# Performance work log

Measured on AMD Instinct MI355X. Metric: run time of the kernel, lower is better.

## Reference

```python
import jax, jax.numpy as jnp
import numpy as np
import math

HID, NH, NKV, HD = 2048, 16, 4, 128
GROUPS = NH // NKV
ROPE_THETA = 10000.0
NBITS = 8


def fake_quant(x, n_bits=NBITS):
    """Per-tensor symmetric min-max fake quantization with STE."""
    qmax = float(2 ** (n_bits - 1) - 1)
    scale = jnp.maximum(jnp.max(jnp.abs(x)) / qmax, jnp.asarray(1e-8, x.dtype))
    q = jnp.clip(jnp.round(x / scale), -qmax - 1.0, qmax) * scale
    return x + jax.lax.stop_gradient(q - x)


def quant_linear(x, w):
    # QuantLinear: fake-quant activation and weight, then x @ w.T
    return jnp.einsum('bsh,oh->bso', fake_quant(x), fake_quant(w))


def rope_cos_sin(position_ids, head_dim, dtype):
    inv_freq = 1.0 / (ROPE_THETA ** (jnp.arange(0, head_dim, 2, dtype=jnp.float32) / head_dim))
    freqs = position_ids.astype(jnp.float32)[..., None] * inv_freq  # [B,S,hd/2]
    emb = jnp.concatenate([freqs, freqs], axis=-1)                   # [B,S,hd]
    return jnp.cos(emb).astype(dtype), jnp.sin(emb).astype(dtype)


def rotate_half(x):
    h = x.shape[-1] // 2
    return jnp.concatenate([-x[..., h:], x[..., :h]], axis=-1)


def setup_inputs() -> dict:
    key = jax.random.key(0)
    ks = jax.random.split(key, 6)
    B, S = 2, 2048
    hidden_states = jax.random.normal(ks[0], (B, S, HID), dtype=jnp.float32)
    neg = jnp.finfo(jnp.float32).min
    causal = jnp.where(jnp.tril(jnp.ones((S, S), dtype=bool)), 0.0, neg).astype(jnp.float32)
    attention_mask = jnp.broadcast_to(causal[None, None], (B, 1, S, S))
    position_ids = jnp.broadcast_to(jnp.arange(S, dtype=jnp.int64)[None], (B, S))
    wq = jax.random.normal(ks[1], (NH * HD, HID), dtype=jnp.float32) * 0.02
    wk = jax.random.normal(ks[2], (NKV * HD, HID), dtype=jnp.float32) * 0.02
    wv = jax.random.normal(ks[3], (NKV * HD, HID), dtype=jnp.float32) * 0.02
    wo = jax.random.normal(ks[4], (HID, NH * HD), dtype=jnp.float32) * 0.02
    return {"hidden_states": hidden_states, "attention_mask": attention_mask,
            "position_ids": position_ids, "wq": wq, "wk": wk, "wv": wv, "wo": wo}


def reference(hidden_states, attention_mask, position_ids, wq, wk, wv, wo):
    B, S, _ = hidden_states.shape
    dtype = hidden_states.dtype
    # quantized projections -> [B, nH, S, hd] / [B, nKV, S, hd]
    q = quant_linear(hidden_states, wq).reshape(B, S, NH, HD).transpose(0, 2, 1, 3)
    k = quant_linear(hidden_states, wk).reshape(B, S, NKV, HD).transpose(0, 2, 1, 3)
    v = quant_linear(hidden_states, wv).reshape(B, S, NKV, HD).transpose(0, 2, 1, 3)
    # RoPE
    cos, sin = rope_cos_sin(position_ids, HD, dtype)
    cos, sin = cos[:, None], sin[:, None]  # broadcast over heads
    q = q * cos + rotate_half(q) * sin
    k = k * cos + rotate_half(k) * sin
    # repeat_kv (GQA)
    k = jnp.repeat(k, GROUPS, axis=1)
    v = jnp.repeat(v, GROUPS, axis=1)
    # fake-quantized QK^T
    q = fake_quant(q)
    k = fake_quant(k)
    attn_weights = jnp.einsum('bhqd,bhkd->bhqk', q, k) / math.sqrt(HD)
    attn_weights = attn_weights + attention_mask
    attn_weights = jnp.maximum(attn_weights, jnp.finfo(attn_weights.dtype).min)
    attn_weights = jax.nn.softmax(attn_weights.astype(jnp.float32), axis=-1).astype(dtype)
    # fake-quantized PV
    p = fake_quant(attn_weights)
    v = fake_quant(v)
    attn_output = jnp.einsum('bhqk,bhkd->bhqd', p, v)
    attn_output = attn_output.transpose(0, 2, 1, 3).reshape(B, S, NH * HD)
    return quant_linear(attn_output, wo)
```

## Files before the change

### kernel.cpp

```cpp
#include <hip/hip_runtime.h>
#include <math.h>
#include <stdint.h>
#include <stddef.h>

#define HID 2048
#define NH 16
#define NKV 4
#define HD 128
#define GROUPS (NH / NKV)
#define BATCH 2
#define SEQ 2048

#define N_HS  8388608ull
#define N_Q   8388608ull
#define N_KV  2097152ull
#define N_WQ  4194304ull
#define N_WKV 1048576ull
#define N_WO  4194304ull

typedef __attribute__((ext_vector_type(8))) short bf16x8;
typedef __attribute__((ext_vector_type(4))) float f32x4;

__device__ inline float quantv(float x, float s) {
  float q = rintf(x / s);
  return fminf(fmaxf(q, -128.0f), 127.0f);
}

__device__ inline float slot_scale(const unsigned int* slots, int i) {
  return fmaxf(__uint_as_float(slots[i]) / 127.0f, 1e-8f);
}

__device__ inline unsigned short f2bf(float x) {
  return (unsigned short)(__float_as_uint(x) >> 16);
}

__device__ inline float amax4(float4 v) {
  return fmaxf(fmaxf(fabsf(v.x), fabsf(v.y)), fmaxf(fabsf(v.z), fabsf(v.w)));
}

__device__ inline void block_amax_atomic(float m, unsigned int* slot) {
  __shared__ float red[256];
  red[threadIdx.x] = m;
  __syncthreads();
  for (int o = 128; o > 0; o >>= 1) {
    if (threadIdx.x < o) red[threadIdx.x] = fmaxf(red[threadIdx.x], red[threadIdx.x + o]);
    __syncthreads();
  }
  if (threadIdx.x == 0) atomicMax(slot, __float_as_uint(red[0]));
}

__device__ __forceinline__ void gload_lds16(const void* g, void* l) {
  __builtin_amdgcn_global_load_lds((const __attribute__((address_space(1))) unsigned int*)g,
                                   (__attribute__((address_space(3))) unsigned int*)l, 16, 0, 0);
}

__global__ __launch_bounds__(256) void absmax5_k(const float* __restrict__ a0,
                                                 const float* __restrict__ a1,
                                                 const float* __restrict__ a2,
                                                 const float* __restrict__ a3,
                                                 const float* __restrict__ a4,
                                                 unsigned int* __restrict__ slots) {
  const int t = blockIdx.y;
  const float* x = t == 0 ? a0 : t == 1 ? a1 : t == 2 ? a2 : t == 3 ? a3 : a4;
  const size_t n4 = (t == 0 ? N_HS : t == 1 ? N_WQ : t == 2 ? N_WKV : t == 3 ? N_WKV : N_WO) / 4;
  const float4* xp = (const float4*)x;
  float m = 0.0f;
  for (size_t i = (size_t)blockIdx.x * 256 + threadIdx.x; i < n4; i += (size_t)gridDim.x * 256)
    m = fmaxf(m, amax4(xp[i]));
  block_amax_atomic(m, slots + t);
}

__global__ __launch_bounds__(256) void quant5_k(const float* __restrict__ a0,
                                                const float* __restrict__ a1,
                                                const float* __restrict__ a2,
                                                const float* __restrict__ a3,
                                                const float* __restrict__ a4,
                                                const unsigned int* __restrict__ slots,
                                                unsigned short* __restrict__ o0,
                                                unsigned short* __restrict__ o1,
                                                unsigned short* __restrict__ o2,
                                                unsigned short* __restrict__ o3,
                                                unsigned short* __restrict__ o4) {
  const int t = blockIdx.y;
  const float* x = t == 0 ? a0 : t == 1 ? a1 : t == 2 ? a2 : t == 3 ? a3 : a4;
  unsigned short* o = t == 0 ? o0 : t == 1 ? o1 : t == 2 ? o2 : t == 3 ? o3 : o4;
  const size_t n4 = (t == 0 ? N_HS : t == 1 ? N_WQ : t == 2 ? N_WKV : t == 3 ? N_WKV : N_WO) / 4;
  const float s = fmaxf(__uint_as_float(slots[t]) / 127.0f, 1e-8f);
  const float4* xp = (const float4*)x;
  ushort4* op = (ushort4*)o;
  for (size_t i = (size_t)blockIdx.x * 256 + threadIdx.x; i < n4; i += (size_t)gridDim.x * 256) {
    float4 v = xp[i];
    ushort4 r;
    r.x = f2bf(quantv(v.x, s));
    r.y = f2bf(quantv(v.y, s));
    r.z = f2bf(quantv(v.z, s));
    r.w = f2bf(quantv(v.w, s));
    op[i] = r;
  }
}

__global__ __launch_bounds__(256) void quant2_k(const float* __restrict__ a0,
                                                const float* __restrict__ a1,
                                                const unsigned int* __restrict__ slots,
                                                unsigned short* __restrict__ o0,
                                                unsigned short* __restrict__ o1) {
  const int t = blockIdx.y;
  const float* x = t == 0 ? a0 : a1;
  unsigned short* o = t == 0 ? o0 : o1;
  const size_t n4 = (t == 0 ? N_Q : N_KV) / 4;
  const float s = fmaxf(__uint_as_float(slots[5 + t]) / 127.0f, 1e-8f);
  const float4* xp = (const float4*)x;
  ushort4* op = (ushort4*)o;
  for (size_t i = (size_t)blockIdx.x * 256 + threadIdx.x; i < n4; i += (size_t)gridDim.x * 256) {
    float4 v = xp[i];
    ushort4 r;
    r.x = f2bf(quantv(v.x, s));
    r.y = f2bf(quantv(v.y, s));
    r.z = f2bf(quantv(v.z, s));
    r.w = f2bf(quantv(v.w, s));
    op[i] = r;
  }
}

__global__ __launch_bounds__(256) void quant1_k(const float* __restrict__ x, size_t n4,
                                                const unsigned int* __restrict__ slot,
                                                unsigned short* __restrict__ out) {
  const float s = fmaxf(__uint_as_float(*slot) / 127.0f, 1e-8f);
  const float4* xp = (const float4*)x;
  ushort4* op = (ushort4*)out;
  for (size_t i = (size_t)blockIdx.x * 256 + threadIdx.x; i < n4; i += (size_t)gridDim.x * 256) {
    float4 v = xp[i];
    ushort4 r;
    r.x = f2bf(quantv(v.x, s));
    r.y = f2bf(quantv(v.y, s));
    r.z = f2bf(quantv(v.z, s));
    r.w = f2bf(quantv(v.w, s));
    op[i] = r;
  }
}

__global__ __launch_bounds__(256) void vtq_k(const float* __restrict__ vbuf,
                                             const unsigned int* __restrict__ slots,
                                             unsigned short* __restrict__ vbt) {
  __shared__ unsigned short L[128 * 72];
  const int tid = threadIdx.x;
  const int s0 = blockIdx.x * 64;
  const int hk = blockIdx.y;
  const int b = blockIdx.z;
  const float s = fmaxf(__uint_as_float(slots[7]) / 127.0f, 1e-8f);
#pragma unroll
  for (int it = 0; it < 8; it++) {
    int idx = tid + it * 256;
    int sl = idx >> 5, c4 = idx & 31;
    float4 v = ((const float4*)(vbuf + ((size_t)(b * SEQ + s0 + sl) * NKV + hk) * HD))[c4];
    L[(c4 * 4 + 0) * 72 + sl] = f2bf(quantv(v.x, s));
    L[(c4 * 4 + 1) * 72 + sl] = f2bf(quantv(v.y, s));
    L[(c4 * 4 + 2) * 72 + sl] = f2bf(quantv(v.z, s));
    L[(c4 * 4 + 3) * 72 + sl] = f2bf(quantv(v.w, s));
  }
  __syncthreads();
  const size_t obase = ((size_t)(b * NKV + hk)) * HD * SEQ + s0;
#pragma unroll
  for (int it = 0; it < 4; it++) {
    int idx = tid + it * 256;
    int d = idx >> 3, sc = idx & 7;
    *(bf16x8*)(vbt + obase + (size_t)d * SEQ + sc * 8) = *(const bf16x8*)(&L[d * 72 + sc * 8]);
  }
}

__device__ __forceinline__ void gemm_body(const unsigned short* __restrict__ A,
                                          const unsigned short* __restrict__ B,
                                          float* __restrict__ C, int N, int K, int m0, int n0,
                                          float sc, int amax_slot, unsigned int* slots) {
  __shared__ unsigned short As[3][128 * 32];
  __shared__ unsigned short Bs[3][128 * 32];
  const int tid = threadIdx.x;
  const int wave = tid >> 6, lane = tid & 63;
  const int l16 = lane & 15, quad = lane >> 4;
  const int wm = (wave & 1) * 64, wn = (wave >> 1) * 64;

  f32x4 acc[4][4];
#pragma unroll
  for (int i = 0; i < 4; i++)
#pragma unroll
    for (int j = 0; j < 4; j++) acc[i][j] = (f32x4){0.f, 0.f, 0.f, 0.f};

  auto STAGE = [&](int buf, int kt) {
#pragma unroll
    for (int it = 0; it < 2; it++) {
      int c = it * 256 + tid;
      int r = c >> 2, kc = (c & 3) * 8;
      gload_lds16(A + (size_t)(m0 + r) * K + kt + kc, &As[buf][(it * 256 + wave * 64) * 8]);
      gload_lds16(B + (size_t)(n0 + r) * K + kt + kc, &Bs[buf][(it * 256 + wave * 64) * 8]);
    }
  };

  const int nk = K / 32;
  STAGE(0, 0);
  STAGE(1, 32);
  STAGE(2, 64);
  for (int t = 0; t < nk; t++) {
    const int buf = t % 3;
    if (t + 3 < nk + 1)      asm volatile("s_waitcnt vmcnt(8)" ::: "memory");
    else if (t + 2 < nk + 1) asm volatile("s_waitcnt vmcnt(4)" ::: "memory");
    else                     asm volatile("s_waitcnt vmcnt(0)" ::: "memory");
    __builtin_amdgcn_sched_barrier(0);
    __builtin_amdgcn_s_barrier();
    __builtin_amdgcn_sched_barrier(0);
    bf16x8 af[4], bq[4];
#pragma unroll
    for (int i = 0; i < 4; i++)
      af[i] = *(const bf16x8*)(&As[buf][(wm + i * 16 + l16) * 32 + quad * 8]);
#pragma unroll
    for (int j = 0; j < 4; j++)
      bq[j] = *(const bf16x8*)(&Bs[buf][(wn + j * 16 + l16) * 32 + quad * 8]);
    asm volatile("s_waitcnt lgkmcnt(0)" ::: "memory");
    __builtin_amdgcn_sched_barrier(0);
    __builtin_amdgcn_s_barrier();
    __builtin_amdgcn_sched_barrier(0);
    if (t + 3 < nk) STAGE(buf, (t + 3) * 32);
#pragma unroll
    for (int i = 0; i < 4; i++)
#pragma unroll
      for (int j = 0; j < 4; j++)
        acc[i][j] = __builtin_amdgcn_mfma_f32_16x16x32_bf16(af[i], bq[j], acc[i][j], 0, 0, 0);
  }

  float am = 0.0f;
#pragma unroll
  for (int i = 0; i < 4; i++)
#pragma unroll
    for (int j = 0; j < 4; j++)
#pragma unroll
      for (int r = 0; r < 4; r++) {
        int row = m0 + wm + i * 16 + quad * 4 + r;
        int col = n0 + wn + j * 16 + l16;
        float v = acc[i][j][r] * sc;
        C[(size_t)row * N + col] = v;
        am = fmaxf(am, fabsf(v));
      }
  if (amax_slot >= 0) {
    __syncthreads();
    float* red = (float*)As;
    red[tid] = am;
    __syncthreads();
    for (int o = 128; o > 0; o >>= 1) {
      if (tid < o) red[tid] = fmaxf(red[tid], red[tid + o]);
      __syncthreads();
    }
    if (tid == 0) atomicMax(slots + amax_slot, __float_as_uint(red[0]));
  }
}

__global__ __launch_bounds__(256) void gemm_qkv_k(const unsigned short* __restrict__ A,
                                                  const unsigned short* __restrict__ Bq,
                                                  const unsigned short* __restrict__ Bk,
                                                  const unsigned short* __restrict__ Bv,
                                                  float* __restrict__ Cq, float* __restrict__ Ck,
                                                  float* __restrict__ Cv,
                                                  unsigned int* __restrict__ slots) {
  const int nt = blockIdx.x, m0 = blockIdx.y * 128;
  const unsigned short* B;
  float* C;
  int N, n0, ib, amx;
  if (nt < 16) {
    B = Bq; C = Cq; N = 2048; n0 = nt * 128; ib = 1; amx = -1;
  } else if (nt < 20) {
    B = Bk; C = Ck; N = 512; n0 = (nt - 16) * 128; ib = 2; amx = -1;
  } else {
    B = Bv; C = Cv; N = 512; n0 = (nt - 20) * 128; ib = 3; amx = 7;
  }
  const float sc = slot_scale(slots, 0) * slot_scale(slots, ib);
  gemm_body(A, B, C, N, HID, m0, n0, sc, amx, slots);
}

__global__ __launch_bounds__(256) void gemm_o_k(const unsigned short* __restrict__ A,
                                                const unsigned short* __restrict__ B,
                                                float* __restrict__ C,
                                                unsigned int* __restrict__ slots) {
  const float sc = slot_scale(slots, 8) * slot_scale(slots, 4);
  gemm_body(A, B, C, HID, NH * HD, blockIdx.y * 128, blockIdx.x * 128, sc, -1, slots);
}

__global__ __launch_bounds__(256) void rope_table_k(float2* __restrict__ tab) {
  int idx = blockIdx.x * 256 + threadIdx.x;
  int i = idx & 63, s = idx >> 6;
  float inv = 1.0f / powf(10000.0f, (float)(2 * i) * (1.0f / 128.0f));
  float fr = (float)s * inv;
  tab[idx] = make_float2(cosf(fr), sinf(fr));
}

__global__ __launch_bounds__(256) void rope_kernel(float* __restrict__ t, int nh, int nhs,
                                                   const float2* __restrict__ tab,
                                                   unsigned int* __restrict__ slot) {
  const size_t total4 = (size_t)BATCH * SEQ * nh * 16;
  float am = 0.0f;
  for (size_t it = (size_t)blockIdx.x * 256 + threadIdx.x; it < total4;
       it += (size_t)gridDim.x * 256) {
    const int i4 = (int)(it & 15);
    const int h = (int)((it >> 4) & (nh - 1));
    const int s = (int)((it >> (4 + nhs)) & (SEQ - 1));
    const int b = (int)(it >> (15 + nhs));
    const size_t base = ((size_t)(b * SEQ + s) * nh + h) * HD + i4 * 4;
    float4 x1 = *(const float4*)(t + base);
    float4 x2 = *(const float4*)(t + base + 64);
    const float4* tp = (const float4*)(tab + (s << 6) + i4 * 4);
    float4 cs01 = tp[0];
    float4 cs23 = tp[1];
    float4 r1, r2;
    r1.x = x1.x * cs01.x - x2.x * cs01.y;  r2.x = x2.x * cs01.x + x1.x * cs01.y;
    r1.y = x1.y * cs01.z - x2.y * cs01.w;  r2.y = x2.y * cs01.z + x1.y * cs01.w;
    r1.z = x1.z * cs23.x - x2.z * cs23.y;  r2.z = x2.z * cs23.x + x1.z * cs23.y;
    r1.w = x1.w * cs23.z - x2.w * cs23.w;  r2.w = x2.w * cs23.z + x1.w * cs23.w;
    *(float4*)(t + base) = r1;
    *(float4*)(t + base + 64) = r2;
    am = fmaxf(am, fmaxf(amax4(r1), amax4(r2)));
  }
  block_amax_atomic(am, slot);
}

#define TK 64
#define KS_STRIDE (HD + 8)
#define VT_STRIDE (TK + 8)
#define PS_STRIDE (TK + 8)

__device__ __forceinline__ void ldK(bf16x8 r[4], const unsigned short* kb, int b, int hk,
                                    int j0, int tid) {
#pragma unroll
  for (int it = 0; it < 4; it++) {
    int c2 = tid + it * 256;
    int rr = c2 >> 4, c = c2 & 15;
    r[it] = *(const bf16x8*)(kb + ((size_t)(b * SEQ + j0 + rr) * NKV + hk) * HD + c * 8);
  }
}
__device__ __forceinline__ void stK(unsigned short* Ks, const bf16x8 r[4], int tid) {
#pragma unroll
  for (int it = 0; it < 4; it++) {
    int c2 = tid + it * 256;
    int rr = c2 >> 4, c = c2 & 15;
    *(bf16x8*)(&Ks[rr * KS_STRIDE + c * 8]) = r[it];
  }
}
__device__ __forceinline__ void ldV(bf16x8 r[4], const unsigned short* vbt, size_t vbase,
                                    int j0, int tid) {
#pragma unroll
  for (int it = 0; it < 4; it++) {
    int idx = tid + it * 256;
    int d = idx >> 3, sc = idx & 7;
    r[it] = *(const bf16x8*)(vbt + vbase + (size_t)d * SEQ + j0 + sc * 8);
  }
}
__device__ __forceinline__ void stV(unsigned short* Vt, const bf16x8 r[4], int tid) {
#pragma unroll
  for (int it = 0; it < 4; it++) {
    int idx = tid + it * 256;
    int d = idx >> 3, sc = idx & 7;
    *(bf16x8*)(&Vt[d * VT_STRIDE + sc * 8]) = r[it];
  }
}

__device__ __forceinline__ void qk4_pair(f32x4 sfrA[4], f32x4 sfrB[4], const unsigned short* Ks,
                                         const bf16x8 qfA[4], const bf16x8 qfB[4], bool doA,
                                         int l16, int quad) {
#pragma unroll
  for (int kt = 0; kt < 4; kt++) {
    f32x4 aA = {0.f, 0.f, 0.f, 0.f}, aB = {0.f, 0.f, 0.f, 0.f};
    const unsigned short* kp = &Ks[(kt * 16 + l16) * KS_STRIDE + quad * 8];
#pragma unroll
    for (int s = 0; s < 4; s++) {
      bf16x8 kf = *(const bf16x8*)(kp + s * 32);
      if (doA) aA = __builtin_amdgcn_mfma_f32_16x16x32_bf16(qfA[s], kf, aA, 0, 0, 0);
      aB = __builtin_amdgcn_mfma_f32_16x16x32_bf16(qfB[s], kf, aB, 0, 0, 0);
    }
    sfrA[kt] = aA;
    sfrB[kt] = aB;
  }
}
__device__ __forceinline__ void lacc(float l[4], const f32x4 sfr[4], float ss, bool diag,
                                     int j0, int qrb, int l16) {
  if (!diag) {
#pragma unroll
    for (int kt = 0; kt < 4; kt++)
#pragma unroll
      for (int r = 0; r < 4; r++) l[r] += __expf(fminf(sfr[kt][r] * ss, 80.0f));
  } else {
#pragma unroll
    for (int kt = 0; kt < 4; kt++) {
      const int key = j0 + kt * 16 + l16;
#pragma unroll
      for (int r = 0; r < 4; r++) {
        float e = __expf(fminf(sfr[kt][r] * ss, 80.0f));
        l[r] += (key <= qrb + r) ? e : 0.0f;
      }
    }
  }
}
__device__ __forceinline__ void pquant(unsigned short* Psb, const f32x4 sfr[4],
                                       const float il[4], float ss, bool diag, int j0,
                                       int qrb, int wave, int l16, int quad) {
  if (!diag) {
#pragma unroll
    for (int kt = 0; kt < 4; kt++)
#pragma unroll
      for (int r = 0; r < 4; r++) {
        float e = __expf(fminf(sfr[kt][r] * ss, 80.0f));
        float p = fminf(rintf(e * il[r]), 127.0f);
        Psb[(wave * 16 + quad * 4 + r) * PS_STRIDE + kt * 16 + l16] = f2bf(p);
      }
  } else {
#pragma unroll
    for (int kt = 0; kt < 4; kt++) {
      const int key = j0 + kt * 16 + l16;
#pragma unroll
      for (int r = 0; r < 4; r++) {
        float e = __expf(fminf(sfr[kt][r] * ss, 80.0f));
        float p = (key <= qrb + r) ? fminf(rintf(e * il[r]), 127.0f) : 0.0f;
        Psb[(wave * 16 + quad * 4 + r) * PS_STRIDE + kt * 16 + l16] = f2bf(p);
      }
    }
  }
}
__device__ __forceinline__ void pvacc_pair(f32x4 ofA[8], f32x4 ofB[8], const unsigned short* Ps,
                                           const unsigned short* Vt, bool doA, int wave,
                                           int l16, int quad) {
  const unsigned short* ppA = &Ps[(wave * 16 + l16) * PS_STRIDE + quad * 8];
  const unsigned short* ppB = ppA + 64 * PS_STRIDE;
  bf16x8 pA0, pA1;
  if (doA) {
    pA0 = *(const bf16x8*)ppA;
    pA1 = *(const bf16x8*)(ppA + 32);
  }
  bf16x8 pB0 = *(const bf16x8*)ppB;
  bf16x8 pB1 = *(const bf16x8*)(ppB + 32);
#pragma unroll
  for (int n = 0; n < 8; n++) {
    const unsigned short* vp = &Vt[(n * 16 + l16) * VT_STRIDE + quad * 8];
    bf16x8 v0 = *(const bf16x8*)vp;
    bf16x8 v1 = *(const bf16x8*)(vp + 32);
    ofB[n] = __builtin_amdgcn_mfma_f32_16x16x32_bf16(pB0, v0, ofB[n], 0, 0, 0);
    ofB[n] = __builtin_amdgcn_mfma_f32_16x16x32_bf16(pB1, v1, ofB[n], 0, 0, 0);
    if (doA) {
      ofA[n] = __builtin_amdgcn_mfma_f32_16x16x32_bf16(pA0, v0, ofA[n], 0, 0, 0);
      ofA[n] = __builtin_amdgcn_mfma_f32_16x16x32_bf16(pA1, v1, ofA[n], 0, 0, 0);
    }
  }
}

__global__ __launch_bounds__(256, 2) void attn_mfma_kernel(const unsigned short* __restrict__ qb,
                                                           const unsigned short* __restrict__ kb,
                                                           const unsigned short* __restrict__ vbt,
                                                           float* __restrict__ ob,
                                                           unsigned int* __restrict__ slots) {
  __shared__ unsigned short Ks[TK * KS_STRIDE];
  __shared__ unsigned short Vt[HD * VT_STRIDE];
  __shared__ unsigned short Ps[128 * PS_STRIDE];

  const int tid = threadIdx.x;
  const int wave = tid >> 6;
  const int lane = tid & 63;
  const int l16 = lane & 15;
  const int quad = lane >> 4;
  const int id = blockIdx.x;
  const int b = (id & 7) >> 2;
  const int hk = id & 3;
  const int j = id >> 3;
  const int h = hk * GROUPS + (j & 3);
  const int slot = j >> 2;
  const int q0A = slot * 64, ntA = slot + 1;
  const int q0B = (31 - slot) * 64, ntB = 32 - slot;

  const float s_q = slot_scale(slots, 5);
  const float s_k = slot_scale(slots, 6);
  const float s_v = slot_scale(slots, 7);
  const float ss = s_q * s_k / 11.313708498984761f;
  const float scale_p = 1.0f / 127.0f;
  const size_t vbase = ((size_t)(b * NKV + hk)) * HD * SEQ;

  bf16x8 qfA[4], qfB[4];
  {
    const unsigned short* qpA =
        qb + ((size_t)(b * SEQ + q0A + wave * 16 + l16) * NH + h) * HD + quad * 8;
    const unsigned short* qpB =
        qb + ((size_t)(b * SEQ + q0B + wave * 16 + l16) * NH + h) * HD + quad * 8;
#pragma unroll
    for (int s = 0; s < 4; s++) {
      qfA[s] = *(const bf16x8*)(qpA + s * 32);
      qfB[s] = *(const bf16x8*)(qpB + s * 32);
    }
  }
  const int qrbA = q0A + wave * 16 + quad * 4;
  const int qrbB = q0B + wave * 16 + quad * 4;

  float lA[4] = {0.f, 0.f, 0.f, 0.f}, lB[4] = {0.f, 0.f, 0.f, 0.f};
  bf16x8 kreg[4];
  ldK(kreg, kb, b, hk, 0, tid);
  for (int t = 0; t < ntB; t++) {
    const int j0 = t * TK;
    __syncthreads();
    stK(Ks, kreg, tid);
    if (t + 1 < ntB) ldK(kreg, kb, b, hk, (t + 1) * TK, tid);
    __syncthreads();
    const bool doA = (t < ntA);
    f32x4 sfrA[4], sfrB[4];
    qk4_pair(sfrA, sfrB, Ks, qfA, qfB, doA, l16, quad);
    if (doA) lacc(lA, sfrA, ss, t == ntA - 1, j0, qrbA, l16);
    lacc(lB, sfrB, ss, t == ntB - 1, j0, qrbB, l16);
  }
  float ilA[4], ilB[4];
#pragma unroll
  for (int r = 0; r < 4; r++) {
#pragma unroll
    for (int off = 1; off < 16; off <<= 1) {
      lA[r] += __shfl_xor(lA[r], off);
      lB[r] += __shfl_xor(lB[r], off);
    }
    ilA[r] = 127.0f / fmaxf(lA[r], 1e-30f);
    ilB[r] = 127.0f / fmaxf(lB[r], 1e-30f);
  }

  f32x4 ofA[8], ofB[8];
#pragma unroll
  for (int n = 0; n < 8; n++) {
    ofA[n] = (f32x4){0.f, 0.f, 0.f, 0.f};
    ofB[n] = (f32x4){0.f, 0.f, 0.f, 0.f};
  }
  bf16x8 vreg[4];
  ldK(kreg, kb, b, hk, 0, tid);
  ldV(vreg, vbt, vbase, 0, tid);
  for (int t = 0; t < ntB; t++) {
    const int j0 = t * TK;
    __syncthreads();
    stK(Ks, kreg, tid);
    stV(Vt, vreg, tid);
    if (t + 1 < ntB) {
      ldK(kreg, kb, b, hk, (t + 1) * TK, tid);
      ldV(vreg, vbt, vbase, (t + 1) * TK, tid);
    }
    __syncthreads();
    const bool doA = (t < ntA);
    f32x4 sfrA[4], sfrB[4];
    qk4_pair(sfrA, sfrB, Ks, qfA, qfB, doA, l16, quad);
    if (doA) pquant(Ps, sfrA, ilA, ss, t == ntA - 1, j0, qrbA, wave, l16, quad);
    pquant(Ps + 64 * PS_STRIDE, sfrB, ilB, ss, t == ntB - 1, j0, qrbB, wave, l16, quad);
    pvacc_pair(ofA, ofB, Ps, Vt, doA, wave, l16, quad);
  }

  const float oscale = scale_p * s_v;
  float amax = 0.0f;
#pragma unroll
  for (int n = 0; n < 8; n++)
#pragma unroll
    for (int r = 0; r < 4; r++) {
      float vA = ofA[n][r] * oscale;
      float vB = ofB[n][r] * oscale;
      ob[((size_t)(b * SEQ + qrbA + r) * NH + h) * HD + n * 16 + l16] = vA;
      ob[((size_t)(b * SEQ + qrbB + r) * NH + h) * HD + n * 16 + l16] = vB;
      amax = fmaxf(amax, fmaxf(fabsf(vA), fabsf(vB)));
    }
  __syncthreads();
  block_amax_atomic(amax, &slots[8]);
}

extern "C" void kernel_launch(void* const* d_in, const int* in_sizes, int n_in,
                              void* d_out, int out_size, void* d_ws, size_t ws_size,
                              hipStream_t stream) {
  const float* hs = (const float*)d_in[0];
  const float* wq = (const float*)d_in[3];
  const float* wk = (const float*)d_in[4];
  const float* wv = (const float*)d_in[5];
  const float* wo = (const float*)d_in[6];
  float* out = (float*)d_out;

  unsigned int* slots = (unsigned int*)d_ws;
  char* p = (char*)d_ws + 256;
  unsigned short* hsq = (unsigned short*)p;  p += 2 * N_HS;
  unsigned short* wqq = (unsigned short*)p;  p += 2 * N_WQ;
  unsigned short* wkq = (unsigned short*)p;  p += 2 * N_WKV;
  unsigned short* wvq = (unsigned short*)p;  p += 2 * N_WKV;
  unsigned short* woq = (unsigned short*)p;  p += 2 * N_WO;
  float* kbuf = (float*)p;                   p += 4 * N_KV;
  float* vbuf = (float*)p;                   p += 4 * N_KV;
  unsigned short* qbf = (unsigned short*)p;  p += 2 * N_Q;
  unsigned short* kbf = (unsigned short*)p;  p += 2 * N_KV;
  unsigned short* vbt = (unsigned short*)p;  p += 2 * N_KV;
  float2* rtab = (float2*)p;
  unsigned short* aobf = hsq;
  float* qbuf = out;
  float* aobuf = out;

  hipMemsetAsync(d_ws, 0, 256, stream);

  rope_table_k<<<(SEQ * 64) / 256, 256, 0, stream>>>(rtab);
  absmax5_k<<<dim3(128, 5), 256, 0, stream>>>(hs, wq, wk, wv, wo, slots);
  quant5_k<<<dim3(128, 5), 256, 0, stream>>>(hs, wq, wk, wv, wo, slots, hsq, wqq, wkq, wvq, woq);

  const int M = BATCH * SEQ;
  gemm_qkv_k<<<dim3(24, M / 128), 256, 0, stream>>>(hsq, wqq, wkq, wvq, qbuf, kbuf, vbuf, slots);

  rope_kernel<<<1024, 256, 0, stream>>>(qbuf, NH, 4, rtab, slots + 5);
  rope_kernel<<<256, 256, 0, stream>>>(kbuf, NKV, 2, rtab, slots + 6);

  quant2_k<<<dim3(128, 2), 256, 0, stream>>>(qbuf, kbuf, slots, qbf, kbf);
  vtq_k<<<dim3(SEQ / 64, NKV, BATCH), 256, 0, stream>>>(vbuf, slots, vbt);

  attn_mfma_kernel<<<dim3(512, 1, 1), 256, 0, stream>>>(qbf, kbf, vbt, aobuf, slots);

  quant1_k<<<256, 256, 0, stream>>>(aobuf, N_Q / 4, slots + 8, aobf);

  gemm_o_k<<<dim3(HID / 128, M / 128), 256, 0, stream>>>(aobf, woq, out, slots);
}
```

Before: 445.2 us.

## Transpose QK MFMA to row-per-lane, fold softmax normalization into exp2 exponent

The QK^T MFMA operands are swapped so each lane holds scores for a single query row. This lets the row sum be a scalar per lane, reduced with two shuffles instead of sixteen. The P computation now uses exp2 with the log-scale and the 1/l factor folded in as an additive log2 term, which removes a multiply. P is written to LDS as packed 4-wide stores. Grid sizes of the absmax, quant and quant2 elementwise kernels are also doubled. Folding the normalization into the exponent may shift rounding slightly, and the clamp-at-127 on P was removed.

```diff
diff --git a/kernel.cpp b/kernel.cpp
--- a/kernel.cpp
+++ b/kernel.cpp
@@ -20,6 +20,9 @@
 
 typedef __attribute__((ext_vector_type(8))) short bf16x8;
 typedef __attribute__((ext_vector_type(4))) float f32x4;
+
+#define LOG2E 1.4426950408889634f
+#define CLAMP_L2 115.41560325f
 
 __device__ inline float quantv(float x, float s) {
   float q = rintf(x / s);
@@ -369,55 +372,56 @@
 #pragma unroll
     for (int s = 0; s < 4; s++) {
       bf16x8 kf = *(const bf16x8*)(kp + s * 32);
-      if (doA) aA = __builtin_amdgcn_mfma_f32_16x16x32_bf16(qfA[s], kf, aA, 0, 0, 0);
-      aB = __builtin_amdgcn_mfma_f32_16x16x32_bf16(qfB[s], kf, aB, 0, 0, 0);
+      if (doA) aA = __builtin_amdgcn_mfma_f32_16x16x32_bf16(kf, qfA[s], aA, 0, 0, 0);
+      aB = __builtin_amdgcn_mfma_f32_16x16x32_bf16(kf, qfB[s], aB, 0, 0, 0);
     }
     sfrA[kt] = aA;
     sfrB[kt] = aB;
   }
 }
-__device__ __forceinline__ void lacc(float l[4], const f32x4 sfr[4], float ss, bool diag,
-                                     int j0, int qrb, int l16) {
+__device__ __forceinline__ void lacc(float& l, const f32x4 sfr[4], float c1, bool diag,
+                                     int j0, int qrow, int quad) {
   if (!diag) {
 #pragma unroll
     for (int kt = 0; kt < 4; kt++)
 #pragma unroll
-      for (int r = 0; r < 4; r++) l[r] += __expf(fminf(sfr[kt][r] * ss, 80.0f));
+      for (int r = 0; r < 4; r++)
+        l += __builtin_amdgcn_exp2f(fminf(sfr[kt][r] * c1, CLAMP_L2));
   } else {
 #pragma unroll
     for (int kt = 0; kt < 4; kt++) {
-      const int key = j0 + kt * 16 + l16;
+      const int key0 = j0 + kt * 16 + quad * 4;
 #pragma unroll
       for (int r = 0; r < 4; r++) {
-        float e = __expf(fminf(sfr[kt][r] * ss, 80.0f));
-        l[r] += (key <= qrb + r) ? e : 0.0f;
+        float e = __builtin_amdgcn_exp2f(fminf(sfr[kt][r] * c1, CLAMP_L2));
+        l += (key0 + r <= qrow) ? e : 0.0f;
       }
     }
   }
 }
 __device__ __forceinline__ void pquant(unsigned short* Psb, const f32x4 sfr[4],
-                                       const float il[4], float ss, bool diag, int j0,
-                                       int qrb, int wave, int l16, int quad) {
-  if (!diag) {
-#pragma unroll
-    for (int kt = 0; kt < 4; kt++)
-#pragma unroll
-      for (int r = 0; r < 4; r++) {
-        float e = __expf(fminf(sfr[kt][r] * ss, 80.0f));
-        float p = fminf(rintf(e * il[r]), 127.0f);
-        Psb[(wave * 16 + quad * 4 + r) * PS_STRIDE + kt * 16 + l16] = f2bf(p);
-      }
-  } else {
-#pragma unroll
-    for (int kt = 0; kt < 4; kt++) {
-      const int key = j0 + kt * 16 + l16;
-#pragma unroll
-      for (int r = 0; r < 4; r++) {
-        float e = __expf(fminf(sfr[kt][r] * ss, 80.0f));
-        float p = (key <= qrb + r) ? fminf(rintf(e * il[r]), 127.0f) : 0.0f;
-        Psb[(wave * 16 + quad * 4 + r) * PS_STRIDE + kt * 16 + l16] = f2bf(p);
-      }
-    }
+                                       float l2il, float c1, bool diag, int j0,
+                                       int qrow, int wave, int l16, int quad) {
+  unsigned short* rowp = &Psb[(wave * 16 + l16) * PS_STRIDE + quad * 4];
+#pragma unroll
+  for (int kt = 0; kt < 4; kt++) {
+    const int key0 = j0 + kt * 16 + quad * 4;
+    float p0 = rintf(__builtin_amdgcn_exp2f(fminf(sfr[kt][0] * c1, CLAMP_L2) + l2il));
+    float p1 = rintf(__builtin_amdgcn_exp2f(fminf(sfr[kt][1] * c1, CLAMP_L2) + l2il));
+    float p2 = rintf(__builtin_amdgcn_exp2f(fminf(sfr[kt][2] * c1, CLAMP_L2) + l2il));
+    float p3 = rintf(__builtin_amdgcn_exp2f(fminf(sfr[kt][3] * c1, CLAMP_L2) + l2il));
+    if (diag) {
+      if (key0 + 0 > qrow) p0 = 0.0f;
+      if (key0 + 1 > qrow) p1 = 0.0f;
+      if (key0 + 2 > qrow) p2 = 0.0f;
+      if (key0 + 3 > qrow) p3 = 0.0f;
+    }
+    ushort4 pk;
+    pk.x = f2bf(p0);
+    pk.y = f2bf(p1);
+    pk.z = f2bf(p2);
+    pk.w = f2bf(p3);
+    *(ushort4*)(rowp + kt * 16) = pk;
   }
 }
 __device__ __forceinline__ void pvacc_pair(f32x4 ofA[8], f32x4 ofB[8], const unsigned short* Ps,
@@ -473,6 +477,7 @@
   const float s_k = slot_scale(slots, 6);
   const float s_v = slot_scale(slots, 7);
   const float ss = s_q * s_k / 11.313708498984761f;
+  const float c1 = ss * LOG2E;
   const float scale_p = 1.0f / 127.0f;
   const size_t vbase = ((size_t)(b * NKV + hk)) * HD * SEQ;
 
@@ -488,10 +493,12 @@
       qfB[s] = *(const bf16x8*)(qpB + s * 32);
     }
   }
+  const int qrowA = q0A + wave * 16 + l16;
+  const int qrowB = q0B + wave * 16 + l16;
   const int qrbA = q0A + wave * 16 + quad * 4;
   const int qrbB = q0B + wave * 16 + quad * 4;
 
-  float lA[4] = {0.f, 0.f, 0.f, 0.f}, lB[4] = {0.f, 0.f, 0.f, 0.f};
+  float lA = 0.f, lB = 0.f;
   bf16x8 kreg[4];
   ldK(kreg, kb, b, hk, 0, tid);
   for (int t = 0; t < ntB; t++) {
@@ -503,20 +510,15 @@
     const bool doA = (t < ntA);
     f32x4 sfrA[4], sfrB[4];
     qk4_pair(sfrA, sfrB, Ks, qfA, qfB, doA, l16, quad);
-    if (doA) lacc(lA, sfrA, ss, t == ntA - 1, j0, qrbA, l16);
-    lacc(lB, sfrB, ss, t == ntB - 1, j0, qrbB, l16);
-  }
-  float ilA[4], ilB[4];
-#pragma unroll
-  for (int r = 0; r < 4; r++) {
-#pragma unroll
-    for (int off = 1; off < 16; off <<= 1) {
-      lA[r] += __shfl_xor(lA[r], off);
-      lB[r] += __shfl_xor(lB[r], off);
-    }
-    ilA[r] = 127.0f / fmaxf(lA[r], 1e-30f);
-    ilB[r] = 127.0f / fmaxf(lB[r], 1e-30f);
-  }
+    if (doA) lacc(lA, sfrA, c1, t == ntA - 1, j0, qrowA, quad);
+    lacc(lB, sfrB, c1, t == ntB - 1, j0, qrowB, quad);
+  }
+  lA += __shfl_xor(lA, 16);
+  lA += __shfl_xor(lA, 32);
+  lB += __shfl_xor(lB, 16);
+  lB += __shfl_xor(lB, 32);
+  const float l2ilA = __log2f(127.0f / fmaxf(lA, 1e-30f));
+  const float l2ilB = __log2f(127.0f / fmaxf(lB, 1e-30f));
 
   f32x4 ofA[8], ofB[8];
 #pragma unroll
@@ -540,8 +542,8 @@
     const bool doA = (t < ntA);
     f32x4 sfrA[4], sfrB[4];
     qk4_pair(sfrA, sfrB, Ks, qfA, qfB, doA, l16, quad);
-    if (doA) pquant(Ps, sfrA, ilA, ss, t == ntA - 1, j0, qrbA, wave, l16, quad);
-    pquant(Ps + 64 * PS_STRIDE, sfrB, ilB, ss, t == ntB - 1, j0, qrbB, wave, l16, quad);
+    if (doA) pquant(Ps, sfrA, l2ilA, c1, t == ntA - 1, j0, qrowA, wave, l16, quad);
+    pquant(Ps + 64 * PS_STRIDE, sfrB, l2ilB, c1, t == ntB - 1, j0, qrowB, wave, l16, quad);
     pvacc_pair(ofA, ofB, Ps, Vt, doA, wave, l16, quad);
   }
 
@@ -591,8 +593,8 @@
   hipMemsetAsync(d_ws, 0, 256, stream);
 
   rope_table_k<<<(SEQ * 64) / 256, 256, 0, stream>>>(rtab);
-  absmax5_k<<<dim3(128, 5), 256, 0, stream>>>(hs, wq, wk, wv, wo, slots);
-  quant5_k<<<dim3(128, 5), 256, 0, stream>>>(hs, wq, wk, wv, wo, slots, hsq, wqq, wkq, wvq, woq);
+  absmax5_k<<<dim3(256, 5), 256, 0, stream>>>(hs, wq, wk, wv, wo, slots);
+  quant5_k<<<dim3(256, 5), 256, 0, stream>>>(hs, wq, wk, wv, wo, slots, hsq, wqq, wkq, wvq, woq);
 
   const int M = BATCH * SEQ;
   gemm_qkv_k<<<dim3(24, M / 128), 256, 0, stream>>>(hsq, wqq, wkq, wvq, qbuf, kbuf, vbuf, slots);
@@ -600,7 +602,7 @@
   rope_kernel<<<1024, 256, 0, stream>>>(qbuf, NH, 4, rtab, slots + 5);
   rope_kernel<<<256, 256, 0, stream>>>(kbuf, NKV, 2, rtab, slots + 6);
 
-  quant2_k<<<dim3(128, 2), 256, 0, stream>>>(qbuf, kbuf, slots, qbf, kbf);
+  quant2_k<<<dim3(256, 2), 256, 0, stream>>>(qbuf, kbuf, slots, qbf, kbf);
   vtq_k<<<dim3(SEQ / 64, NKV, BATCH), 256, 0, stream>>>(vbuf, slots, vbt);
 
   attn_mfma_kernel<<<dim3(512, 1, 1), 256, 0, stream>>>(qbf, kbf, vbt, aobuf, slots);
```

Result: faster. 416.4 us (-6.5%).
